# Kernel tuning notes

Measured on AMD Instinct MI355X. Metric: run time of the kernel, lower is better.

## Reference

```python
import jax, jax.numpy as jnp
import numpy as np

N = 40000      # nodes
E = 640000     # edges
D = 128        # embed_dim
H = 8          # heads
DH = D // H    # per-head dim
L = 3          # n_layers
IN = 64        # in_dim
FF = 218       # embed_dim2 (ffn hidden)
OUT = 1        # out_dim
EPS = 1e-5
NEG_SLOPE = 0.2


def setup_inputs() -> dict:
    key = jax.random.key(0)
    ks = jax.random.split(key, 16)
    nrm = lambda k, shape, s=0.1: (jax.random.normal(k, shape, jnp.float32) * s)
    return {
        "x": jax.random.normal(ks[0], (N, IN), jnp.float32),
        "src": jax.random.randint(ks[1], (E,), 0, N, jnp.int32),
        "dst": jax.random.randint(ks[2], (E,), 0, N, jnp.int32),
        "W_emb": nrm(ks[3], (IN, D)),
        "b_emb": jnp.zeros((D,), jnp.float32),
        "gat_W": nrm(ks[4], (L, D, D)),
        "attn_l": nrm(ks[5], (L, H, DH)),
        "attn_r": nrm(ks[6], (L, H, DH)),
        "gat_b": jnp.zeros((L, D), jnp.float32),
        "bn1_g": jnp.ones((L, D), jnp.float32),
        "bn1_b": jnp.zeros((L, D), jnp.float32),
        "ff_W1": nrm(ks[7], (L, D, FF)),
        "ff_b1": jnp.zeros((L, FF), jnp.float32),
        "ff_W2": nrm(ks[8], (L, FF, D)),
        "ff_b2": jnp.zeros((L, D), jnp.float32),
        "bn2_g": jnp.ones((L, D), jnp.float32),
        "bn2_b": jnp.zeros((L, D), jnp.float32),
        "dec_W1": nrm(ks[9], ((L + 1) * D, D)),
        "dec_bn_g": jnp.ones((D,), jnp.float32),
        "dec_bn_b": jnp.zeros((D,), jnp.float32),
        "dec_W2": nrm(ks[10], (D, OUT)),
    }


def _batchnorm(h, g, b):
    # BatchNorm1d in training mode: batch stats over nodes, biased variance
    mu = h.mean(axis=0)
    var = h.var(axis=0)
    return g * (h - mu) * jax.lax.rsqrt(var + EPS) + b


def _gat_layer(h, src, dst, W, al, ar, bias):
    n = h.shape[0]
    feat = (h @ W).reshape(n, H, DH)                      # [N,H,DH]
    el = (feat * al).sum(-1)                               # [N,H]
    er = (feat * ar).sum(-1)                               # [N,H]
    e = jax.nn.leaky_relu(el[src] + er[dst], NEG_SLOPE)    # [E,H]
    # segment softmax over incoming edges of each dst node
    emax = jax.ops.segment_max(e, dst, num_segments=n)
    ex = jnp.exp(e - emax[dst])
    den = jax.ops.segment_sum(ex, dst, num_segments=n)
    alpha = ex / den[dst]                                  # [E,H]
    msg = alpha[:, :, None] * feat[src]                    # [E,H,DH]
    out = jax.ops.segment_sum(msg, dst, num_segments=n)    # [N,H,DH]
    out = out + bias.reshape(H, DH)
    return out.reshape(n, D)


def reference(x, src, dst, W_emb, b_emb, gat_W, attn_l, attn_r, gat_b,
              bn1_g, bn1_b, ff_W1, ff_b1, ff_W2, ff_b2, bn2_g, bn2_b,
              dec_W1, dec_bn_g, dec_bn_b, dec_W2):
    h = x @ W_emb + b_emb                                  # embed_layer
    xs = [h]
    for l in range(L):
        # message passing with skip connection
        h = h + _gat_layer(h, src, dst, gat_W[l], attn_l[l], attn_r[l], gat_b[l])
        # feed forward: BN -> Skip(Linear,ReLU,Linear) -> BN
        h = _batchnorm(h, bn1_g[l], bn1_b[l])
        y = jax.nn.relu(h @ ff_W1[l] + ff_b1[l]) @ ff_W2[l] + ff_b2[l]
        h = _batchnorm(h + y, bn2_g[l], bn2_b[l])
        xs.append(h)
    h = jnp.concatenate(xs, axis=-1)                       # JumpingKnowledge 'cat'
    # decision MLP: relu(BN(h W1)) W2, no biases
    h = jax.nn.relu(_batchnorm(h @ dec_W1, dec_bn_g, dec_bn_b))
    return h @ dec_W2
```

## Files before the change

kernel.cpp:

```cpp
#include <hip/hip_runtime.h>
#include <hip/hip_bf16.h>
#include <math.h>

#define N_NODES 40000
#define N_EDGES 640000
#define DIM     128
#define HEADS   8
#define DHEAD   16
#define LAYERS  3
#define IN_DIM  64
#define FF_DIM  218
#define BN_EPS  1e-5f
#define NEG_SLOPE 0.2f
#define INV_N   (1.f / N_NODES)
#define NREP    128

typedef __attribute__((ext_vector_type(8))) short  bhalf8;
typedef __attribute__((ext_vector_type(4))) float  floatx4;
typedef __attribute__((ext_vector_type(4))) int    intx4;

__device__ __forceinline__ unsigned bfpack2(float a, float b) {
    unsigned ua = __float_as_uint(a);
    ua = ua + 0x7FFFu + ((ua >> 16) & 1u);
    unsigned ub = __float_as_uint(b);
    ub = ub + 0x7FFFu + ((ub >> 16) & 1u);
    return (ua >> 16) | (ub & 0xFFFF0000u);
}
__device__ __forceinline__ unsigned short bf16of(float a) {
    unsigned ua = __float_as_uint(a);
    ua = ua + 0x7FFFu + ((ua >> 16) & 1u);
    return (unsigned short)(ua >> 16);
}
__device__ __forceinline__ float bf2f(unsigned short u) {
    return __uint_as_float(((unsigned)u) << 16);
}
__device__ __forceinline__ float bflo(unsigned u) { return __uint_as_float(u << 16); }
__device__ __forceinline__ float bfhi(unsigned u) { return __uint_as_float(u & 0xFFFF0000u); }
__device__ __forceinline__ float rsum16(float v) {
    v += __shfl_xor(v, 1, 16);
    v += __shfl_xor(v, 2, 16);
    v += __shfl_xor(v, 4, 16);
    v += __shfl_xor(v, 8, 16);
    return v;
}

#define OFF_EMB 0
#define OFF_GAT 8192
#define OFF_W1  57344
#define OFF_W2  143360
#define OFF_DEC 229376
#define WPK_TOT 294912
#define HIST_BLOCKS ((N_EDGES + 255) / 256)
#define PACK_BLOCKS ((WPK_TOT + 255) / 256)

__global__ void hist_pack_kernel(const int* __restrict__ dst, int* __restrict__ counts,
                                 const float* __restrict__ W_emb,
                                 const float* __restrict__ gat_W,
                                 const float* __restrict__ ff_W1,
                                 const float* __restrict__ ff_W2,
                                 const float* __restrict__ dec_W1,
                                 unsigned short* __restrict__ wpk) {
    int bid = blockIdx.x;
    if (bid < HIST_BLOCKS) {
        int e = bid * 256 + threadIdx.x;
        if (e < N_EDGES) atomicAdd(&counts[dst[e]], 1);
        return;
    }
    int i = (bid - HIST_BLOCKS) * 256 + threadIdx.x;
    if (i >= WPK_TOT) return;
    int o = i;
    if (o < 8192) {
        int n = o >> 6, k = o & 63;
        wpk[OFF_EMB + o] = bf16of(W_emb[k * 128 + n]);
        return;
    }
    o -= 8192;
    if (o < 3 * 16384) {
        int l = o >> 14, r = o & 16383;
        int n = r >> 7, k = r & 127;
        wpk[OFF_GAT + o] = bf16of(gat_W[l * 16384 + k * 128 + n]);
        return;
    }
    o -= 3 * 16384;
    if (o < 3 * 28672) {
        int l = o / 28672, r = o % 28672;
        int n = r >> 7, k = r & 127;
        float v = (n < FF_DIM) ? ff_W1[(size_t)l * 128 * FF_DIM + k * FF_DIM + n] : 0.f;
        wpk[OFF_W1 + o] = bf16of(v);
        return;
    }
    o -= 3 * 28672;
    if (o < 3 * 28672) {
        int l = o / 28672, r = o % 28672;
        int n = r / 224, k = r % 224;
        float v = (k < FF_DIM) ? ff_W2[(size_t)l * FF_DIM * 128 + k * 128 + n] : 0.f;
        wpk[OFF_W2 + o] = bf16of(v);
        return;
    }
    o -= 3 * 28672;
    {
        int n = o >> 9, k = o & 511;
        wpk[OFF_DEC + o] = bf16of(dec_W1[k * 128 + n]);
    }
}

__global__ __launch_bounds__(1024) void scan_kernel(const int* __restrict__ counts,
                                                    int* __restrict__ indptr,
                                                    int* __restrict__ cursor, int n) {
    __shared__ int tsum[1024];
    const int CH = 40;
    int tid = threadIdx.x;
    int base = tid * CH;
    int loc[CH];
    int s = 0;
    #pragma unroll
    for (int i = 0; i < CH; i++) {
        int idx = base + i;
        int v = (idx < n) ? counts[idx] : 0;
        loc[i] = s;
        s += v;
    }
    tsum[tid] = s;
    __syncthreads();
    for (int offs = 1; offs < 1024; offs <<= 1) {
        int t = (tid >= offs) ? tsum[tid - offs] : 0;
        __syncthreads();
        tsum[tid] += t;
        __syncthreads();
    }
    int carry = (tid > 0) ? tsum[tid - 1] : 0;
    #pragma unroll
    for (int i = 0; i < CH; i++) {
        int idx = base + i;
        if (idx < n) {
            int v = carry + loc[i];
            indptr[idx] = v;
            cursor[idx] = v;
        }
    }
    if (tid == 1023) indptr[n] = tsum[1023];
}

__global__ void scatter_kernel(const int* __restrict__ src, const int* __restrict__ dst,
                               int* __restrict__ cursor,
                               int* __restrict__ srcs_csr) {
    int e = blockIdx.x * blockDim.x + threadIdx.x;
    if (e < N_EDGES) {
        int d = dst[e];
        int pos = atomicAdd(&cursor[d], 1);
        srcs_csr[pos] = src[e];
    }
}

template<int NT, int KPAD, int AMODE, bool ABF16, int MT, bool ELER, bool RESBF>
__global__ __launch_bounds__(256) void gemm_l2_kernel(
    const float* __restrict__ A, const unsigned short* __restrict__ Abf, int lda,
    const unsigned short* __restrict__ Bpk,
    const float* __restrict__ bias,
    const void* __restrict__ resv, int ldres,
    const float* __restrict__ res_stats, const float* __restrict__ res_g,
    const float* __restrict__ res_b,
    float* __restrict__ C, unsigned short* __restrict__ Cbf, int ldc,
    float* __restrict__ out_stats,
    int M, int Nact, int relu,
    const float* __restrict__ a_stats, float* __restrict__ a_stats_out,
    const float* __restrict__ a_g, const float* __restrict__ a_b,
    const float* __restrict__ al, const float* __restrict__ ar,
    float* __restrict__ el_out, float* __restrict__ er_out)
{
    constexpr int SCN = (AMODE > 0) ? KPAD : 1;
    constexpr int BROWS = 64 * MT;
    constexpr int STEPS = KPAD / 32;
    constexpr int CST = (STEPS > 2) ? 2 : STEPS;
    __shared__ float sc_s[SCN];
    __shared__ float sh_s[SCN];
    __shared__ float st_sum[128];
    __shared__ float st_sq[128];
    __shared__ float el_s[ELER ? BROWS : 1][ELER ? NT : 1];
    __shared__ float er_s[ELER ? BROWS : 1][ELER ? NT : 1];

    int tid = threadIdx.x, wave = tid >> 6, lane = tid & 63;
    int q = lane >> 4, tl = lane & 15;
    int colbase = blockIdx.y * (NT * 16);
    int row0b = blockIdx.x * BROWS;
    int rowtile = row0b + wave * (MT * 16);

    if constexpr (AMODE == 1 || AMODE == 2) {
        for (int idx = tid; idx < KPAD; idx += 256) {
            float scv = 1.f, shv = 0.f;
            if constexpr (AMODE == 1) {
                float mu = a_stats[idx] * INV_N;
                float var = a_stats[128 + idx] * INV_N - mu * mu;
                scv = a_g[idx] * rsqrtf(var + BN_EPS);
                shv = a_b[idx] - mu * scv;
            } else {
                int l = idx >> 7;
                if (l > 0) {
                    int c = idx & 127;
                    const float* st = a_stats + (l - 1) * 256;
                    float mu = st[c] * INV_N;
                    float var = st[128 + c] * INV_N - mu * mu;
                    scv = a_g[(l - 1) * 128 + c] * rsqrtf(var + BN_EPS);
                    shv = a_b[(l - 1) * 128 + c] - mu * scv;
                }
            }
            sc_s[idx] = scv;
            sh_s[idx] = shv;
        }
        __syncthreads();
    }
    if constexpr (AMODE == 3) {
        for (int idx = tid; idx < 128; idx += 256) {
            float s = 0.f, sq = 0.f;
            #pragma unroll 8
            for (int r = 0; r < NREP; r++) {
                s  += a_stats[r * 256 + idx];
                sq += a_stats[r * 256 + 128 + idx];
            }
            a_stats_out[idx] = s;
            a_stats_out[128 + idx] = sq;
            float mu = s * INV_N;
            float var = sq * INV_N - mu * mu;
            float scv = a_g[idx] * rsqrtf(var + BN_EPS);
            sc_s[idx] = scv;
            sh_s[idx] = a_b[idx] - mu * scv;
        }
        __syncthreads();
    }

    int rowm[MT];
    bool vrm[MT];
    #pragma unroll
    for (int mt = 0; mt < MT; mt++) {
        rowm[mt] = rowtile + mt * 16 + tl;
        vrm[mt] = rowm[mt] < M;
    }
    const unsigned short* bp = Bpk + (size_t)colbase * KPAD;

    floatx4 acc[MT][NT] = {};

    #pragma unroll
    for (int c0 = 0; c0 < STEPS; c0 += CST) {
        intx4  arawb[CST][MT];
        floatx4 araw0[ABF16 ? 1 : CST][ABF16 ? 1 : MT];
        floatx4 araw1[ABF16 ? 1 : CST][ABF16 ? 1 : MT];
        bhalf8 breg[CST][NT];
        #pragma unroll
        for (int cs = 0; cs < CST; cs++) {
            if (c0 + cs >= STEPS) continue;
            int gk = (c0 + cs) * 32 + q * 8;
            #pragma unroll
            for (int j = 0; j < NT; j++)
                breg[cs][j] = *(const bhalf8*)(bp + (size_t)(j * 16 + tl) * KPAD + gk);
            #pragma unroll
            for (int mt = 0; mt < MT; mt++) {
                if constexpr (ABF16) {
                    intx4 u = {};
                    if (vrm[mt]) u = *(const intx4*)(Abf + (size_t)rowm[mt] * lda + gk);
                    arawb[cs][mt] = u;
                } else {
                    floatx4 x0 = {}, x1 = {};
                    if (vrm[mt]) {
                        const float* ap = A + (size_t)rowm[mt] * lda + gk;
                        x0 = *(const floatx4*)ap;
                        x1 = *(const floatx4*)(ap + 4);
                    }
                    araw0[cs][mt] = x0;
                    araw1[cs][mt] = x1;
                }
            }
        }
        #pragma unroll
        for (int cs = 0; cs < CST; cs++) {
            if (c0 + cs >= STEPS) continue;
            int gk = (c0 + cs) * 32 + q * 8;
            bhalf8 af[MT];
            #pragma unroll
            for (int mt = 0; mt < MT; mt++) {
                if constexpr (ABF16) {
                    intx4 u = arawb[cs][mt];
                    if constexpr (AMODE > 0) {
                        #pragma unroll
                        for (int w = 0; w < 4; w++) {
                            unsigned uw = (unsigned)u[w];
                            float lo = bflo(uw), hi = bfhi(uw);
                            lo = fmaf(sc_s[gk + 2 * w],     lo, sh_s[gk + 2 * w]);
                            hi = fmaf(sc_s[gk + 2 * w + 1], hi, sh_s[gk + 2 * w + 1]);
                            u[w] = (int)bfpack2(lo, hi);
                        }
                    }
                    af[mt] = *(bhalf8*)&u;
                } else {
                    floatx4 x0 = araw0[cs][mt], x1 = araw1[cs][mt];
                    if constexpr (AMODE > 0) {
                        #pragma unroll
                        for (int jj = 0; jj < 4; jj++) {
                            x0[jj] = fmaf(sc_s[gk + jj],     x0[jj], sh_s[gk + jj]);
                            x1[jj] = fmaf(sc_s[gk + 4 + jj], x1[jj], sh_s[gk + 4 + jj]);
                        }
                    }
                    intx4 t = intx4{(int)bfpack2(x0[0], x0[1]), (int)bfpack2(x0[2], x0[3]),
                                    (int)bfpack2(x1[0], x1[1]), (int)bfpack2(x1[2], x1[3])};
                    af[mt] = *(bhalf8*)&t;
                }
            }
            #pragma unroll
            for (int mt = 0; mt < MT; mt++)
                #pragma unroll
                for (int j = 0; j < NT; j++)
                    acc[mt][j] = __builtin_amdgcn_mfma_f32_16x16x32_bf16(af[mt], breg[cs][j], acc[mt][j], 0, 0, 0);
        }
    }

    float psum[NT], psq[NT];
    #pragma unroll
    for (int j = 0; j < NT; j++) { psum[j] = 0.f; psq[j] = 0.f; }

    #pragma unroll
    for (int j = 0; j < NT; j++) {
        int c = colbase + j * 16 + tl;
        bool cok = c < Nact;
        float bv = (bias && cok) ? bias[c] : 0.f;
        float rsc = 1.f, rsh = 0.f;
        if (res_stats && cok) {
            float mu = res_stats[c] * INV_N;
            float var = res_stats[128 + c] * INV_N - mu * mu;
            rsc = res_g[c] * rsqrtf(var + BN_EPS);
            rsh = res_b[c] - mu * rsc;
        }
        float alc = 0.f, arc = 0.f;
        if constexpr (ELER) { alc = al[c]; arc = ar[c]; }
        #pragma unroll
        for (int mt = 0; mt < MT; mt++) {
            #pragma unroll
            for (int reg = 0; reg < 4; reg++) {
                int r = rowtile + mt * 16 + q * 4 + reg;
                bool rok = r < M;
                float v = 0.f;
                if (rok && cok) {
                    v = acc[mt][j][reg] + bv;
                    if (resv) {
                        size_t ri = (size_t)r * ldres + c;
                        float rv = RESBF ? bf2f(((const unsigned short*)resv)[ri])
                                         : ((const float*)resv)[ri];
                        v = fmaf(rsc, rv, v + rsh);
                    }
                    if (relu) v = fmaxf(v, 0.f);
                    if (out_stats) { psum[j] += v; psq[j] = fmaf(v, v, psq[j]); }
                }
                if constexpr (ELER) {
                    float pel = rsum16(v * alc);
                    float per_ = rsum16(v * arc);
                    if (tl == 0) {
                        int rl = wave * (MT * 16) + mt * 16 + q * 4 + reg;
                        el_s[rl][j] = pel;
                        er_s[rl][j] = per_;
                    }
                }
                if (rok) {
                    if (Cbf) Cbf[(size_t)r * ldc + c] = bf16of(v);
                    else if (cok) C[(size_t)r * ldc + c] = v;
                }
            }
        }
    }

    if constexpr (ELER) {
        __syncthreads();
        int gh = blockIdx.y * NT;
        for (int idx = tid; idx < BROWS * NT; idx += 256) {
            int rl = idx / NT, hj = idx % NT;
            int r = row0b + rl;
            if (r < M) {
                el_out[(size_t)r * 8 + gh + hj] = el_s[rl][hj];
                er_out[(size_t)r * 8 + gh + hj] = er_s[rl][hj];
            }
        }
    }

    if (out_stats) {
        __syncthreads();
        if (tid < 128) { st_sum[tid] = 0.f; st_sq[tid] = 0.f; }
        __syncthreads();
        #pragma unroll
        for (int j = 0; j < NT; j++) {
            int c = colbase + j * 16 + tl;
            if (c < 128) { atomicAdd(&st_sum[c], psum[j]); atomicAdd(&st_sq[c], psq[j]); }
        }
        __syncthreads();
        if (tid < 128) {
            atomicAdd(&out_stats[tid], st_sum[tid]);
            atomicAdd(&out_stats[128 + tid], st_sq[tid]);
        }
    }
}

__global__ __launch_bounds__(256) void gat_aggregate_kernel(
    const unsigned short* __restrict__ feat,
    const float* __restrict__ el, const float* __restrict__ er,
    const int* __restrict__ indptr, const int* __restrict__ srcs_csr,
    const unsigned short* __restrict__ h_in, int ldh,
    const float* __restrict__ hstats, const float* __restrict__ hg,
    const float* __restrict__ hb,
    const float* __restrict__ bias,
    unsigned short* __restrict__ outp,
    float* __restrict__ stats_rep)
{
    int n = blockIdx.x;
    int t = threadIdx.x;
    int p = t >> 6;
    int lane = t & 63;
    int d0 = lane * 2;
    int hh = lane >> 3;
    int pick = lane & 3;
    int gb = lane & 56;
    __shared__ float red[4][128];
    __shared__ float denh[4][HEADS];
    int beg = indptr[n], end = indptr[n + 1];
    float ern = er[(size_t)n * 8 + hh];

    float acc0 = 0.f, acc1 = 0.f, den = 0.f;
    int i = beg + p;
    for (; i + 12 < end; i += 16) {
        int s0 = srcs_csr[i],     s1 = srcs_csr[i + 4];
        int s2 = srcs_csr[i + 8], s3 = srcs_csr[i + 12];
        int sp = pick == 0 ? s0 : pick == 1 ? s1 : pick == 2 ? s2 : s3;
        float ee = el[(size_t)sp * 8 + hh] + ern;
        unsigned f0 = *(const unsigned*)(feat + (size_t)s0 * DIM + d0);
        unsigned f1 = *(const unsigned*)(feat + (size_t)s1 * DIM + d0);
        unsigned f2 = *(const unsigned*)(feat + (size_t)s2 * DIM + d0);
        unsigned f3 = *(const unsigned*)(feat + (size_t)s3 * DIM + d0);
        float aa = expf(ee > 0.f ? ee : NEG_SLOPE * ee);
        float a0 = __shfl(aa, gb + 0);
        float a1 = __shfl(aa, gb + 1);
        float a2 = __shfl(aa, gb + 2);
        float a3 = __shfl(aa, gb + 3);
        den += (a0 + a1) + (a2 + a3);
        acc0 = fmaf(a0, bflo(f0), acc0); acc1 = fmaf(a0, bfhi(f0), acc1);
        acc0 = fmaf(a1, bflo(f1), acc0); acc1 = fmaf(a1, bfhi(f1), acc1);
        acc0 = fmaf(a2, bflo(f2), acc0); acc1 = fmaf(a2, bfhi(f2), acc1);
        acc0 = fmaf(a3, bflo(f3), acc0); acc1 = fmaf(a3, bfhi(f3), acc1);
    }
    for (; i < end; i += 4) {
        int s0 = srcs_csr[i];
        float e0 = el[(size_t)s0 * 8 + hh] + ern;
        unsigned f0 = *(const unsigned*)(feat + (size_t)s0 * DIM + d0);
        float a0 = expf(e0 > 0.f ? e0 : NEG_SLOPE * e0);
        den += a0;
        acc0 = fmaf(a0, bflo(f0), acc0);
        acc1 = fmaf(a0, bfhi(f0), acc1);
    }
    red[p][d0] = acc0;
    red[p][d0 + 1] = acc1;
    if ((lane & 7) == 0) denh[p][hh] = den;
    __syncthreads();
    if (t < 128) {
        int d = t, h = d >> 4;
        float tot = (red[0][d] + red[1][d]) + (red[2][d] + red[3][d]);
        float dtot = (denh[0][h] + denh[1][h]) + (denh[2][h] + denh[3][h]);
        float inv = dtot > 0.f ? 1.f / dtot : 0.f;
        float hv = bf2f(h_in[(size_t)n * ldh + d]);
        if (hstats) {
            float mu = hstats[d] * INV_N;
            float var = hstats[128 + d] * INV_N - mu * mu;
            float s = hg[d] * rsqrtf(var + BN_EPS);
            hv = fmaf(s, hv - mu, hb[d]);
        }
        unsigned short ub = bf16of(hv + tot * inv + bias[d]);
        outp[(size_t)n * DIM + d] = ub;
        float vr = bf2f(ub);
        float* rep = stats_rep + ((size_t)(n & (NREP - 1)) << 8);
        atomicAdd(&rep[d], vr);
        atomicAdd(&rep[128 + d], vr * vr);
    }
}

__global__ __launch_bounds__(256) void decide_kernel(
    const unsigned short* __restrict__ z, const float* __restrict__ stats,
    const float* __restrict__ g, const float* __restrict__ b,
    const float* __restrict__ W2, float* __restrict__ outp, int M)
{
    int wid = threadIdx.x >> 6, lane = threadIdx.x & 63;
    int n = blockIdx.x * 4 + wid;
    if (n >= M) return;
    float acc = 0.f;
    #pragma unroll
    for (int cc = 0; cc < 2; cc++) {
        int c = lane + cc * 64;
        float mu  = stats[c] * INV_N;
        float var = stats[DIM + c] * INV_N - mu * mu;
        float v = fmaf(g[c] * rsqrtf(var + BN_EPS), bf2f(z[(size_t)n * DIM + c]) - mu, b[c]);
        v = fmaxf(v, 0.f);
        acc = fmaf(v, W2[c], acc);
    }
    #pragma unroll
    for (int offs = 32; offs > 0; offs >>= 1)
        acc += __shfl_down(acc, offs);
    if (lane == 0) outp[n] = acc;
}

extern "C" void kernel_launch(void* const* d_in, const int* in_sizes, int n_in,
                              void* d_out, int out_size, void* d_ws, size_t ws_size,
                              hipStream_t stream)
{
    const float* x      = (const float*)d_in[0];
    const int*   src    = (const int*)  d_in[1];
    const int*   dst    = (const int*)  d_in[2];
    const float* W_emb  = (const float*)d_in[3];
    const float* b_emb  = (const float*)d_in[4];
    const float* gat_W  = (const float*)d_in[5];
    const float* attn_l = (const float*)d_in[6];
    const float* attn_r = (const float*)d_in[7];
    const float* gat_b  = (const float*)d_in[8];
    const float* bn1_g  = (const float*)d_in[9];
    const float* bn1_b  = (const float*)d_in[10];
    const float* ff_W1  = (const float*)d_in[11];
    const float* ff_b1  = (const float*)d_in[12];
    const float* ff_W2  = (const float*)d_in[13];
    const float* ff_b2  = (const float*)d_in[14];
    const float* bn2_g  = (const float*)d_in[15];
    const float* bn2_b  = (const float*)d_in[16];
    const float* dec_W1 = (const float*)d_in[17];
    const float* dec_bn_g = (const float*)d_in[18];
    const float* dec_bn_b = (const float*)d_in[19];
    const float* dec_W2 = (const float*)d_in[20];
    float* outp = (float*)d_out;

    char* ws = (char*)d_ws;
    size_t off = 0;
    auto alloc = [&](size_t bytes) -> void* {
        void* p = ws + off;
        off += (bytes + 255) & ~(size_t)255;
        return p;
    };
    unsigned short* xsb = (unsigned short*)alloc((size_t)N_NODES * 512 * 2);
    unsigned short* zb  = (unsigned short*)alloc((size_t)N_NODES * DIM * 2);
    unsigned short* featb = (unsigned short*)alloc((size_t)N_NODES * DIM * 2);
    float* el    = (float*)alloc((size_t)N_NODES * HEADS * 4);
    float* er    = (float*)alloc((size_t)N_NODES * HEADS * 4);
    unsigned short* y1b = (unsigned short*)alloc((size_t)N_NODES * 224 * 2);
    unsigned short* btb = (unsigned short*)alloc((size_t)N_NODES * DIM * 2);
    int*   counts= (int*)  alloc((size_t)N_NODES * 4);
    float* statsAll = (float*)alloc(((size_t)3 * NREP * 256 + 7 * 256) * 4);
    unsigned short* wpk = (unsigned short*)alloc((size_t)WPK_TOT * 2);
    int*   indptr= (int*)  alloc((size_t)(N_NODES + 1) * 4);
    int*   cursor= (int*)  alloc((size_t)N_NODES * 4);
    int*   srcs_csr = (int*)alloc((size_t)N_EDGES * 4);
    (void)ws_size; (void)in_sizes; (void)n_in; (void)out_size;

    float* rep1   = statsAll;
    float* stats1c= statsAll + 3 * NREP * 256;
    float* stats2 = statsAll + 3 * NREP * 256 + 3 * 256;
    float* statsD = statsAll + 3 * NREP * 256 + 6 * 256;

    dim3 gg2((N_NODES + 127) / 128, 2);

    hipMemsetAsync(counts, 0, (size_t)N_NODES * 4 + ((size_t)3 * NREP * 256 + 7 * 256) * 4, stream);
    hist_pack_kernel<<<HIST_BLOCKS + PACK_BLOCKS, 256, 0, stream>>>(
        dst, counts, W_emb, gat_W, ff_W1, ff_W2, dec_W1, wpk);
    scan_kernel<<<1, 1024, 0, stream>>>(counts, indptr, cursor, N_NODES);
    scatter_kernel<<<(N_EDGES + 255) / 256, 256, 0, stream>>>(src, dst, cursor, srcs_csr);

    gemm_l2_kernel<4, 64, 0, false, 2, false, false><<<gg2, 256, 0, stream>>>(
        x, nullptr, IN_DIM, wpk + OFF_EMB, b_emb,
        nullptr, 0, nullptr, nullptr, nullptr,
        nullptr, xsb, 512, nullptr,
        N_NODES, DIM, 0, nullptr, nullptr, nullptr, nullptr,
        nullptr, nullptr, nullptr, nullptr);

    for (int l = 0; l < LAYERS; l++) {
        const unsigned short* h_cur = xsb + (size_t)l * DIM;
        const float* hstats = l ? stats2 + (l - 1) * 256 : nullptr;
        const float* hg = l ? bn2_g + (l - 1) * DIM : nullptr;
        const float* hb = l ? bn2_b + (l - 1) * DIM : nullptr;
        if (l == 0)
            gemm_l2_kernel<4, 128, 0, true, 2, true, false><<<gg2, 256, 0, stream>>>(
                nullptr, h_cur, 512, wpk + OFF_GAT + l * 16384, nullptr,
                nullptr, 0, nullptr, nullptr, nullptr,
                nullptr, featb, DIM, nullptr,
                N_NODES, DIM, 0, nullptr, nullptr, nullptr, nullptr,
                attn_l + l * DIM, attn_r + l * DIM, el, er);
        else
            gemm_l2_kernel<4, 128, 1, true, 2, true, false><<<gg2, 256, 0, stream>>>(
                nullptr, h_cur, 512, wpk + OFF_GAT + l * 16384, nullptr,
                nullptr, 0, nullptr, nullptr, nullptr,
                nullptr, featb, DIM, nullptr,
                N_NODES, DIM, 0, hstats, nullptr, hg, hb,
                attn_l + l * DIM, attn_r + l * DIM, el, er);
        gat_aggregate_kernel<<<N_NODES, 256, 0, stream>>>(
            featb, el, er, indptr, srcs_csr, h_cur, 512,
            hstats, hg, hb, gat_b + l * DIM, btb,
            rep1 + (size_t)l * NREP * 256);
        gemm_l2_kernel<7, 128, 3, true, 2, false, false><<<gg2, 256, 0, stream>>>(
            nullptr, btb, DIM, wpk + OFF_W1 + l * 28672,
            ff_b1 + l * FF_DIM,
            nullptr, 0, nullptr, nullptr, nullptr,
            nullptr, y1b, 224, nullptr,
            N_NODES, FF_DIM, 1,
            rep1 + (size_t)l * NREP * 256, stats1c + l * 256,
            bn1_g + l * DIM, bn1_b + l * DIM,
            nullptr, nullptr, nullptr, nullptr);
        gemm_l2_kernel<4, 224, 0, true, 2, false, true><<<gg2, 256, 0, stream>>>(
            nullptr, y1b, 224, wpk + OFF_W2 + l * 28672,
            ff_b2 + l * DIM,
            btb, DIM, stats1c + l * 256, bn1_g + l * DIM, bn1_b + l * DIM,
            nullptr, xsb + (size_t)(l + 1) * DIM, 512, stats2 + l * 256,
            N_NODES, DIM, 0, nullptr, nullptr, nullptr, nullptr,
            nullptr, nullptr, nullptr, nullptr);
    }

    gemm_l2_kernel<4, 512, 2, true, 2, false, false><<<gg2, 256, 0, stream>>>(
        nullptr, xsb, 512, wpk + OFF_DEC, nullptr,
        nullptr, 0, nullptr, nullptr, nullptr,
        nullptr, zb, DIM, statsD,
        N_NODES, DIM, 0, stats2, nullptr, bn2_g, bn2_b,
        nullptr, nullptr, nullptr, nullptr);
    decide_kernel<<<(N_NODES + 3) / 4, 256, 0, stream>>>(
        zb, statsD, dec_bn_g, dec_bn_b, dec_W2, outp, N_NODES);
}
```

Before: 782.3 us.

## Split GEMM K dimension across waves with LDS reduction of partial accumulators

Replaces the row-tiled GEMM, where each of the 4 waves owned its own 32 rows, with a split-K scheme. All 4 waves now share one 32-row tile and each handles a quarter of the K steps. Partial accumulators are reduced through shared memory in two stages, and wave 0 runs the epilogue (bias, residual BN, relu, stats, el/er). This launches 4x more blocks and shortens per-wave K loops, trading extra LDS traffic, three barriers and a single-wave epilogue for more parallelism and latency hiding.

```diff
diff --git a/kernel.cpp b/kernel.cpp
--- a/kernel.cpp
+++ b/kernel.cpp
@@ -152,8 +152,8 @@
     }
 }
 
-template<int NT, int KPAD, int AMODE, bool ABF16, int MT, bool ELER, bool RESBF>
-__global__ __launch_bounds__(256) void gemm_l2_kernel(
+template<int NT, int KPAD, int AMODE, bool ABF16, bool ELER, bool RESBF>
+__global__ __launch_bounds__(256) void gemm_sk_kernel(
     const float* __restrict__ A, const unsigned short* __restrict__ Abf, int lda,
     const unsigned short* __restrict__ Bpk,
     const float* __restrict__ bias,
@@ -168,22 +168,25 @@
     const float* __restrict__ al, const float* __restrict__ ar,
     float* __restrict__ el_out, float* __restrict__ er_out)
 {
+    constexpr int MT = 2;
     constexpr int SCN = (AMODE > 0) ? KPAD : 1;
-    constexpr int BROWS = 64 * MT;
     constexpr int STEPS = KPAD / 32;
-    constexpr int CST = (STEPS > 2) ? 2 : STEPS;
+    constexpr int SH = (STEPS + 3) / 4;
+    constexpr int CSTk = (SH > 2) ? 2 : SH;
     __shared__ float sc_s[SCN];
     __shared__ float sh_s[SCN];
     __shared__ float st_sum[128];
     __shared__ float st_sq[128];
-    __shared__ float el_s[ELER ? BROWS : 1][ELER ? NT : 1];
-    __shared__ float er_s[ELER ? BROWS : 1][ELER ? NT : 1];
+    __shared__ float part[2][MT * NT * 4][64];
+    __shared__ float el_s[ELER ? 32 : 1][ELER ? NT : 1];
+    __shared__ float er_s[ELER ? 32 : 1][ELER ? NT : 1];
 
     int tid = threadIdx.x, wave = tid >> 6, lane = tid & 63;
     int q = lane >> 4, tl = lane & 15;
     int colbase = blockIdx.y * (NT * 16);
-    int row0b = blockIdx.x * BROWS;
-    int rowtile = row0b + wave * (MT * 16);
+    int rowtile = blockIdx.x * 32;
+
+    if (out_stats && tid < 128) { st_sum[tid] = 0.f; st_sq[tid] = 0.f; }
 
     if constexpr (AMODE == 1 || AMODE == 2) {
         for (int idx = tid; idx < KPAD; idx += 256) {
@@ -238,17 +241,24 @@
     const unsigned short* bp = Bpk + (size_t)colbase * KPAD;
 
     floatx4 acc[MT][NT] = {};
+    int sbeg = wave * SH;
 
     #pragma unroll
-    for (int c0 = 0; c0 < STEPS; c0 += CST) {
-        intx4  arawb[CST][MT];
-        floatx4 araw0[ABF16 ? 1 : CST][ABF16 ? 1 : MT];
-        floatx4 araw1[ABF16 ? 1 : CST][ABF16 ? 1 : MT];
-        bhalf8 breg[CST][NT];
-        #pragma unroll
-        for (int cs = 0; cs < CST; cs++) {
-            if (c0 + cs >= STEPS) continue;
-            int gk = (c0 + cs) * 32 + q * 8;
+    for (int c0o = 0; c0o < SH; c0o += CSTk) {
+        intx4  arawb[CSTk][MT];
+        floatx4 araw0[ABF16 ? 1 : CSTk][ABF16 ? 1 : MT];
+        floatx4 araw1[ABF16 ? 1 : CSTk][ABF16 ? 1 : MT];
+        bhalf8 breg[CSTk][NT];
+        bool actv[CSTk];
+        int gks[CSTk];
+        #pragma unroll
+        for (int cs = 0; cs < CSTk; cs++) {
+            if (c0o + cs >= SH) { actv[cs] = false; gks[cs] = q * 8; continue; }
+            int s = sbeg + c0o + cs;
+            bool act = s < STEPS;
+            actv[cs] = act;
+            int gk = (act ? s : 0) * 32 + q * 8;
+            gks[cs] = gk;
             #pragma unroll
             for (int j = 0; j < NT; j++)
                 breg[cs][j] = *(const bhalf8*)(bp + (size_t)(j * 16 + tl) * KPAD + gk);
@@ -256,11 +266,11 @@
             for (int mt = 0; mt < MT; mt++) {
                 if constexpr (ABF16) {
                     intx4 u = {};
-                    if (vrm[mt]) u = *(const intx4*)(Abf + (size_t)rowm[mt] * lda + gk);
+                    if (act && vrm[mt]) u = *(const intx4*)(Abf + (size_t)rowm[mt] * lda + gk);
                     arawb[cs][mt] = u;
                 } else {
                     floatx4 x0 = {}, x1 = {};
-                    if (vrm[mt]) {
+                    if (act && vrm[mt]) {
                         const float* ap = A + (size_t)rowm[mt] * lda + gk;
                         x0 = *(const floatx4*)ap;
                         x1 = *(const floatx4*)(ap + 4);
@@ -271,9 +281,10 @@
             }
         }
         #pragma unroll
-        for (int cs = 0; cs < CST; cs++) {
-            if (c0 + cs >= STEPS) continue;
-            int gk = (c0 + cs) * 32 + q * 8;
+        for (int cs = 0; cs < CSTk; cs++) {
+            if (c0o + cs >= SH) continue;
+            if (!actv[cs]) continue;
+            int gk = gks[cs];
             bhalf8 af[MT];
             #pragma unroll
             for (int mt = 0; mt < MT; mt++) {
@@ -312,87 +323,126 @@
         }
     }
 
-    float psum[NT], psq[NT];
-    #pragma unroll
-    for (int j = 0; j < NT; j++) { psum[j] = 0.f; psq[j] = 0.f; }
-
-    #pragma unroll
-    for (int j = 0; j < NT; j++) {
-        int c = colbase + j * 16 + tl;
-        bool cok = c < Nact;
-        float bv = (bias && cok) ? bias[c] : 0.f;
-        float rsc = 1.f, rsh = 0.f;
-        if (res_stats && cok) {
-            float mu = res_stats[c] * INV_N;
-            float var = res_stats[128 + c] * INV_N - mu * mu;
-            rsc = res_g[c] * rsqrtf(var + BN_EPS);
-            rsh = res_b[c] - mu * rsc;
-        }
-        float alc = 0.f, arc = 0.f;
-        if constexpr (ELER) { alc = al[c]; arc = ar[c]; }
-        #pragma unroll
-        for (int mt = 0; mt < MT; mt++) {
-            #pragma unroll
-            for (int reg = 0; reg < 4; reg++) {
-                int r = rowtile + mt * 16 + q * 4 + reg;
-                bool rok = r < M;
-                float v = 0.f;
-                if (rok && cok) {
-                    v = acc[mt][j][reg] + bv;
-                    if (resv) {
-                        size_t ri = (size_t)r * ldres + c;
-                        float rv = RESBF ? bf2f(((const unsigned short*)resv)[ri])
-                                         : ((const float*)resv)[ri];
-                        v = fmaf(rsc, rv, v + rsh);
+    #define PIDX(mt, j, reg) ((mt) * NT * 4 + (j) * 4 + (reg))
+    if (wave >= 2) {
+        int slot = wave - 2;
+        #pragma unroll
+        for (int mt = 0; mt < MT; mt++)
+            #pragma unroll
+            for (int j = 0; j < NT; j++)
+                #pragma unroll
+                for (int reg = 0; reg < 4; reg++)
+                    part[slot][PIDX(mt, j, reg)][lane] = acc[mt][j][reg];
+    }
+    __syncthreads();
+    if (wave < 2) {
+        #pragma unroll
+        for (int mt = 0; mt < MT; mt++)
+            #pragma unroll
+            for (int j = 0; j < NT; j++)
+                #pragma unroll
+                for (int reg = 0; reg < 4; reg++)
+                    acc[mt][j][reg] += part[wave][PIDX(mt, j, reg)][lane];
+    }
+    __syncthreads();
+    if (wave == 1) {
+        #pragma unroll
+        for (int mt = 0; mt < MT; mt++)
+            #pragma unroll
+            for (int j = 0; j < NT; j++)
+                #pragma unroll
+                for (int reg = 0; reg < 4; reg++)
+                    part[0][PIDX(mt, j, reg)][lane] = acc[mt][j][reg];
+    }
+    __syncthreads();
+
+    if (wave == 0) {
+        #pragma unroll
+        for (int mt = 0; mt < MT; mt++)
+            #pragma unroll
+            for (int j = 0; j < NT; j++)
+                #pragma unroll
+                for (int reg = 0; reg < 4; reg++)
+                    acc[mt][j][reg] += part[0][PIDX(mt, j, reg)][lane];
+
+        float psum[NT], psq[NT];
+        #pragma unroll
+        for (int j = 0; j < NT; j++) { psum[j] = 0.f; psq[j] = 0.f; }
+
+        #pragma unroll
+        for (int j = 0; j < NT; j++) {
+            int c = colbase + j * 16 + tl;
+            bool cok = c < Nact;
+            float bv = (bias && cok) ? bias[c] : 0.f;
+            float rsc = 1.f, rsh = 0.f;
+            if (res_stats && cok) {
+                float mu = res_stats[c] * INV_N;
+                float var = res_stats[128 + c] * INV_N - mu * mu;
+                rsc = res_g[c] * rsqrtf(var + BN_EPS);
+                rsh = res_b[c] - mu * rsc;
+            }
+            float alc = 0.f, arc = 0.f;
+            if constexpr (ELER) { alc = al[c]; arc = ar[c]; }
+            #pragma unroll
+            for (int mt = 0; mt < MT; mt++) {
+                #pragma unroll
+                for (int reg = 0; reg < 4; reg++) {
+                    int r = rowtile + mt * 16 + q * 4 + reg;
+                    bool rok = r < M;
+                    float v = 0.f;
+                    if (rok && cok) {
+                        v = acc[mt][j][reg] + bv;
+                        if (resv) {
+                            size_t ri = (size_t)r * ldres + c;
+                            float rv = RESBF ? bf2f(((const unsigned short*)resv)[ri])
+                                             : ((const float*)resv)[ri];
+                            v = fmaf(rsc, rv, v + rsh);
+                        }
+                        if (relu) v = fmaxf(v, 0.f);
+                        if (out_stats) { psum[j] += v; psq[j] = fmaf(v, v, psq[j]); }
                     }
-                    if (relu) v = fmaxf(v, 0.f);
-                    if (out_stats) { psum[j] += v; psq[j] = fmaf(v, v, psq[j]); }
-                }
-                if constexpr (ELER) {
-                    float pel = rsum16(v * alc);
-                    float per_ = rsum16(v * arc);
-                    if (tl == 0) {
-                        int rl = wave * (MT * 16) + mt * 16 + q * 4 + reg;
-                        el_s[rl][j] = pel;
-                        er_s[rl][j] = per_;
+                    if constexpr (ELER) {
+                        float pel = rsum16(v * alc);
+                        float per_ = rsum16(v * arc);
+                        if (tl == 0) {
+                            int rl = mt * 16 + q * 4 + reg;
+                            el_s[rl][j] = pel;
+                            er_s[rl][j] = per_;
+                        }
+                    }
+                    if (rok) {
+                        if (Cbf) Cbf[(size_t)r * ldc + c] = bf16of(v);
+                        else if (cok) C[(size_t)r * ldc + c] = v;
                     }
                 }
-                if (rok) {
-                    if (Cbf) Cbf[(size_t)r * ldc + c] = bf16of(v);
-                    else if (cok) C[(size_t)r * ldc + c] = v;
-                }
-            }
-        }
-    }
-
+            }
+        }
+        if (out_stats) {
+            #pragma unroll
+            for (int j = 0; j < NT; j++) {
+                int c = colbase + j * 16 + tl;
+                if (c < 128) { atomicAdd(&st_sum[c], psum[j]); atomicAdd(&st_sq[c], psq[j]); }
+            }
+        }
+    }
+
+    if (ELER || out_stats) __syncthreads();
     if constexpr (ELER) {
-        __syncthreads();
         int gh = blockIdx.y * NT;
-        for (int idx = tid; idx < BROWS * NT; idx += 256) {
+        for (int idx = tid; idx < 32 * NT; idx += 256) {
             int rl = idx / NT, hj = idx % NT;
-            int r = row0b + rl;
+            int r = rowtile + rl;
             if (r < M) {
                 el_out[(size_t)r * 8 + gh + hj] = el_s[rl][hj];
                 er_out[(size_t)r * 8 + gh + hj] = er_s[rl][hj];
             }
         }
     }
-
-    if (out_stats) {
-        __syncthreads();
-        if (tid < 128) { st_sum[tid] = 0.f; st_sq[tid] = 0.f; }
-        __syncthreads();
-        #pragma unroll
-        for (int j = 0; j < NT; j++) {
-            int c = colbase + j * 16 + tl;
-            if (c < 128) { atomicAdd(&st_sum[c], psum[j]); atomicAdd(&st_sq[c], psq[j]); }
-        }
-        __syncthreads();
-        if (tid < 128) {
-            atomicAdd(&out_stats[tid], st_sum[tid]);
-            atomicAdd(&out_stats[128 + tid], st_sq[tid]);
-        }
-    }
+    if (out_stats && tid < 128) {
+        atomicAdd(&out_stats[tid], st_sum[tid]);
+        atomicAdd(&out_stats[128 + tid], st_sq[tid]);
+    }
+    #undef PIDX
 }
 
 __global__ __launch_bounds__(256) void gat_aggregate_kernel(
@@ -553,7 +603,7 @@
     float* stats2 = statsAll + 3 * NREP * 256 + 3 * 256;
     float* statsD = statsAll + 3 * NREP * 256 + 6 * 256;
 
-    dim3 gg2((N_NODES + 127) / 128, 2);
+    dim3 ggs((N_NODES + 31) / 32, 2);
 
     hipMemsetAsync(counts, 0, (size_t)N_NODES * 4 + ((size_t)3 * NREP * 256 + 7 * 256) * 4, stream);
     hist_pack_kernel<<<HIST_BLOCKS + PACK_BLOCKS, 256, 0, stream>>>(
@@ -561,7 +611,7 @@
     scan_kernel<<<1, 1024, 0, stream>>>(counts, indptr, cursor, N_NODES);
     scatter_kernel<<<(N_EDGES + 255) / 256, 256, 0, stream>>>(src, dst, cursor, srcs_csr);
 
-    gemm_l2_kernel<4, 64, 0, false, 2, false, false><<<gg2, 256, 0, stream>>>(
+    gemm_sk_kernel<4, 64, 0, false, false, false><<<ggs, 256, 0, stream>>>(
         x, nullptr, IN_DIM, wpk + OFF_EMB, b_emb,
         nullptr, 0, nullptr, nullptr, nullptr,
         nullptr, xsb, 512, nullptr,
@@ -574,14 +624,14 @@
         const float* hg = l ? bn2_g + (l - 1) * DIM : nullptr;
         const float* hb = l ? bn2_b + (l - 1) * DIM : nullptr;
         if (l == 0)
-            gemm_l2_kernel<4, 128, 0, true, 2, true, false><<<gg2, 256, 0, stream>>>(
+            gemm_sk_kernel<4, 128, 0, true, true, false><<<ggs, 256, 0, stream>>>(
                 nullptr, h_cur, 512, wpk + OFF_GAT + l * 16384, nullptr,
                 nullptr, 0, nullptr, nullptr, nullptr,
                 nullptr, featb, DIM, nullptr,
                 N_NODES, DIM, 0, nullptr, nullptr, nullptr, nullptr,
                 attn_l + l * DIM, attn_r + l * DIM, el, er);
         else
-            gemm_l2_kernel<4, 128, 1, true, 2, true, false><<<gg2, 256, 0, stream>>>(
+            gemm_sk_kernel<4, 128, 1, true, true, false><<<ggs, 256, 0, stream>>>(
                 nullptr, h_cur, 512, wpk + OFF_GAT + l * 16384, nullptr,
                 nullptr, 0, nullptr, nullptr, nullptr,
                 nullptr, featb, DIM, nullptr,
@@ -591,7 +641,7 @@
             featb, el, er, indptr, srcs_csr, h_cur, 512,
             hstats, hg, hb, gat_b + l * DIM, btb,
             rep1 + (size_t)l * NREP * 256);
-        gemm_l2_kernel<7, 128, 3, true, 2, false, false><<<gg2, 256, 0, stream>>>(
+        gemm_sk_kernel<7, 128, 3, true, false, false><<<ggs, 256, 0, stream>>>(
             nullptr, btb, DIM, wpk + OFF_W1 + l * 28672,
             ff_b1 + l * FF_DIM,
             nullptr, 0, nullptr, nullptr, nullptr,
@@ -600,7 +650,7 @@
             rep1 + (size_t)l * NREP * 256, stats1c + l * 256,
             bn1_g + l * DIM, bn1_b + l * DIM,
             nullptr, nullptr, nullptr, nullptr);
-        gemm_l2_kernel<4, 224, 0, true, 2, false, true><<<gg2, 256, 0, stream>>>(
+        gemm_sk_kernel<4, 224, 0, true, false, true><<<ggs, 256, 0, stream>>>(
             nullptr, y1b, 224, wpk + OFF_W2 + l * 28672,
             ff_b2 + l * DIM,
             btb, DIM, stats1c + l * 256, bn1_g + l * DIM, bn1_b + l * DIM,
@@ -609,7 +659,7 @@
             nullptr, nullptr, nullptr, nullptr);
     }
 
-    gemm_l2_kernel<4, 512, 2, true, 2, false, false><<<gg2, 256, 0, stream>>>(
+    gemm_sk_kernel<4, 512, 2, true, false, false><<<ggs, 256, 0, stream>>>(
         nullptr, xsb, 512, wpk + OFF_DEC, nullptr,
         nullptr, 0, nullptr, nullptr, nullptr,
         nullptr, zb, DIM, statsD,
```

After: 1.166 ms. 1.49x slower.
